# Performance work log

Hardware: AMD Instinct MI355X
Metric: run time of the kernel (lower is better)

The kernel has to match this reference:

```python
import jax, jax.numpy as jnp
import numpy as np

DEPTH = 2; C = 96; DIN = 192; R = 6; N = 16; K = 4
B = 1; H0 = 64; W0 = 64; L0 = H0 * W0


def layer_norm(x, g, b, eps=1e-5):
    m = jnp.mean(x, -1, keepdims=True)
    v = jnp.var(x, -1, keepdims=True)
    return (x - m) / jnp.sqrt(v + eps) * g + b


def selective_scan(u, delta, A, Bs, Cs, D):
    # u, delta: (B, KD, L); A: (KD, N); Bs, Cs: (B, K, N, L); D: (KD,)
    Bb, KD, L = u.shape
    Kk = Bs.shape[1]; Dd = KD // Kk; Nn = A.shape[1]
    dA = jnp.exp(delta[..., None] * A[None, :, None, :])              # (B,KD,L,N)
    Bfull = jnp.broadcast_to(Bs[:, :, None], (Bb, Kk, Dd, Nn, L)).reshape(Bb, KD, Nn, L)
    Cfull = jnp.broadcast_to(Cs[:, :, None], (Bb, Kk, Dd, Nn, L)).reshape(Bb, KD, Nn, L)
    dBu = delta[..., None] * Bfull.transpose(0, 1, 3, 2) * u[..., None]  # (B,KD,L,N)
    Ct = Cfull.transpose(3, 0, 1, 2)                                   # (L,B,KD,N)

    def step(h, inp):
        dA_t, dBu_t, C_t = inp
        h = dA_t * h + dBu_t
        return h, jnp.sum(h * C_t, -1)

    init = jnp.zeros((Bb, KD, Nn), u.dtype)
    _, ys = jax.lax.scan(step, init, (dA.transpose(2, 0, 1, 3), dBu.transpose(2, 0, 1, 3), Ct))
    y = ys.transpose(1, 2, 0)                                          # (B,KD,L)
    return y + D[None, :, None] * u


def ss2d(x, in_proj_w, conv_w, conv_b, x_proj_w, dt_w, dt_b, A_logs, Ds, outn_g, outn_b, out_proj_w):
    # x: (B,H,W,C)
    Bb, H, W, Cc = x.shape
    L = H * W
    xz = x @ in_proj_w.T                                  # (B,H,W,2*DIN)
    Din = xz.shape[-1] // 2
    xc, z = xz[..., :Din], xz[..., Din:]
    xc = xc.transpose(0, 3, 1, 2)                         # (B,DIN,H,W)
    xc = jax.lax.conv_general_dilated(xc, conv_w, (1, 1), 'SAME',
                                      feature_group_count=Din,
                                      dimension_numbers=('NCHW', 'OIHW', 'NCHW'))
    xc = jax.nn.silu(xc + conv_b[None, :, None, None])
    # cross-scan: 4 directions
    x0 = xc.reshape(Bb, Din, L)
    x1 = xc.transpose(0, 1, 3, 2).reshape(Bb, Din, L)
    xs = jnp.stack([x0, x1, jnp.flip(x0, -1), jnp.flip(x1, -1)], 1)  # (B,K,DIN,L)
    x_dbl = jnp.einsum('bkdl,kcd->bkcl', xs, x_proj_w)
    dts, Bm, Cm = x_dbl[:, :, :R], x_dbl[:, :, R:R + N], x_dbl[:, :, R + N:]
    dts = jnp.einsum('bkrl,kdr->bkdl', dts, dt_w)
    u = xs.reshape(Bb, K * Din, L)
    delta = jax.nn.softplus(dts.reshape(Bb, K * Din, L) + dt_b.reshape(K * Din)[None, :, None])
    A = -jnp.exp(A_logs)                                  # (K*DIN, N)
    ys = selective_scan(u, delta, A, Bm, Cm, Ds).reshape(Bb, K, Din, L)
    # cross-merge
    y0 = ys[:, 0]
    y1 = ys[:, 1].reshape(Bb, Din, W, H).transpose(0, 1, 3, 2).reshape(Bb, Din, L)
    y2 = jnp.flip(ys[:, 2], -1)
    y3 = jnp.flip(ys[:, 3], -1).reshape(Bb, Din, W, H).transpose(0, 1, 3, 2).reshape(Bb, Din, L)
    y = (y0 + y1 + y2 + y3).transpose(0, 2, 1).reshape(Bb, H, W, Din)
    y = layer_norm(y, outn_g, outn_b)
    y = y * jax.nn.silu(z)
    return y @ out_proj_w.T                               # (B,H,W,C)


def setup_inputs() -> dict:
    key = jax.random.key(0)
    ks = jax.random.split(key, 10)
    f = jnp.float32
    rn = lambda k, s: jax.random.normal(k, s, f) * 0.02
    return {
        'x': jax.random.normal(ks[0], (B, L0, C), f),
        'H': H0, 'W': W0,
        'norm1_g': jnp.ones((DEPTH, C), f), 'norm1_b': jnp.zeros((DEPTH, C), f),
        'vssn_g': jnp.ones((DEPTH, C), f), 'vssn_b': jnp.zeros((DEPTH, C), f),
        'in_proj_w': rn(ks[1], (DEPTH, 2 * DIN, C)),
        'conv_w': rn(ks[2], (DEPTH, DIN, 1, 3, 3)),
        'conv_b': jnp.zeros((DEPTH, DIN), f),
        'x_proj_w': rn(ks[3], (DEPTH, K, R + 2 * N, DIN)),
        'dt_w': rn(ks[4], (DEPTH, K, DIN, R)),
        'dt_b': jax.random.uniform(ks[5], (DEPTH, K, DIN), f, -4.0, -2.0),
        'A_logs': jnp.log(jnp.broadcast_to(jnp.arange(1, N + 1, dtype=f), (DEPTH, K * DIN, N))),
        'Ds': jnp.ones((DEPTH, K * DIN), f),
        'outn_g': jnp.ones((DEPTH, DIN), f), 'outn_b': jnp.zeros((DEPTH, DIN), f),
        'out_proj_w': rn(ks[6], (DEPTH, C, DIN)),
        'res_conv_w': rn(ks[7], (C, C, 3, 3)),
        'res_conv_b': jnp.zeros((C,), f),
    }


def reference(x, H, W, norm1_g, norm1_b, vssn_g, vssn_b, in_proj_w, conv_w, conv_b,
              x_proj_w, dt_w, dt_b, A_logs, Ds, outn_g, outn_b, out_proj_w,
              res_conv_w, res_conv_b):
    Bb, Ll, Cc = x.shape
    shortcut = x
    for i in range(DEPTH):
        sc = x
        xn = layer_norm(x, norm1_g[i], norm1_b[i]).reshape(Bb, H, W, Cc)
        # VSSBlock: internal pre-norm + residual around SS2D (drop_path = 0)
        xi = xn + ss2d(layer_norm(xn, vssn_g[i], vssn_b[i]), in_proj_w[i], conv_w[i],
                       conv_b[i], x_proj_w[i], dt_w[i], dt_b[i], A_logs[i], Ds[i],
                       outn_g[i], outn_b[i], out_proj_w[i])
        x = sc + xi.reshape(Bb, Ll, Cc)
    xc = x.transpose(0, 2, 1).reshape(Bb, Cc, H, W)
    xc = jax.lax.conv_general_dilated(xc, res_conv_w, (1, 1), 'SAME',
                                      dimension_numbers=('NCHW', 'OIHW', 'NCHW'))
    xc = xc + res_conv_b[None, :, None, None]
    return xc.reshape(Bb, Cc, Ll).transpose(0, 2, 1) + shortcut
```

## Files before the change

### kernel.cpp

```cpp
#include <hip/hip_runtime.h>
#include <math.h>

#define LTOK 4096
#define CCH  96
#define DIN_ 192
#define KDIR 4
#define NST  16
#define KD_  768

#define O_XN     0
#define O_XZ     786432
#define O_XCONV  2359296
#define O_XCONVT 3145728
#define O_DELTA  3932160
#define O_BM     7077888
#define O_CM     7340032
#define O_YS     9961472
#define O_XCUR   13107200

__device__ __forceinline__ float siluf(float x) { return x / (1.f + __expf(-x)); }

__global__ void fusedA_kernel(const float* __restrict__ x, const float* __restrict__ g1,
                              const float* __restrict__ b1, const float* __restrict__ g2,
                              const float* __restrict__ b2, const float* __restrict__ w,
                              float* __restrict__ xn, float* __restrict__ xz) {
  __shared__ float As[96 * 72];
  __shared__ float Bs[96 * 68];
  int tid = threadIdx.x;
  int l0 = blockIdx.x * 64;
  int j0 = blockIdx.y * 64;
  int m = tid >> 2, j = tid & 3;
  int l = l0 + m;
  float v[24];
  float s = 0.f, ss = 0.f;
#pragma unroll
  for (int t = 0; t < 24; ++t) {
    int k = j + 4 * t;
    float vv = x[l * 96 + k];
    v[t] = vv; s += vv; ss += vv * vv;
  }
  s += __shfl_xor(s, 1); ss += __shfl_xor(ss, 1);
  s += __shfl_xor(s, 2); ss += __shfl_xor(ss, 2);
  float m1 = s * (1.f / 96.f);
  float rs1 = rsqrtf(ss * (1.f / 96.f) - m1 * m1 + 1e-5f);
  float s2 = 0.f, ss2 = 0.f;
#pragma unroll
  for (int t = 0; t < 24; ++t) {
    int k = j + 4 * t;
    float nv = (v[t] - m1) * rs1 * g1[k] + b1[k];
    v[t] = nv; s2 += nv; ss2 += nv * nv;
    if (blockIdx.y == 0) xn[l * 96 + k] = nv;
  }
  s2 += __shfl_xor(s2, 1); ss2 += __shfl_xor(ss2, 1);
  s2 += __shfl_xor(s2, 2); ss2 += __shfl_xor(ss2, 2);
  float m2 = s2 * (1.f / 96.f);
  float rs2 = rsqrtf(ss2 * (1.f / 96.f) - m2 * m2 + 1e-5f);
#pragma unroll
  for (int t = 0; t < 24; ++t) {
    int k = j + 4 * t;
    As[k * 72 + m] = (v[t] - m2) * rs2 * g2[k] + b2[k];
  }
  for (int qi = tid; qi < 64 * 24; qi += 256) {
    int nn = qi / 24, q = qi % 24;
    const float4 wv = *(const float4*)&w[(j0 + nn) * 96 + q * 4];
    Bs[(q * 4 + 0) * 68 + nn] = wv.x;
    Bs[(q * 4 + 1) * 68 + nn] = wv.y;
    Bs[(q * 4 + 2) * 68 + nn] = wv.z;
    Bs[(q * 4 + 3) * 68 + nn] = wv.w;
  }
  __syncthreads();
  int mg = tid & 15, ng = tid >> 4;
  float acc[4][4] = {};
  for (int k = 0; k < 96; ++k) {
    float a0 = As[k * 72 + 4 * mg + 0], a1 = As[k * 72 + 4 * mg + 1];
    float a2 = As[k * 72 + 4 * mg + 2], a3 = As[k * 72 + 4 * mg + 3];
    float b0 = Bs[k * 68 + 4 * ng + 0], b1_ = Bs[k * 68 + 4 * ng + 1];
    float b2_ = Bs[k * 68 + 4 * ng + 2], b3 = Bs[k * 68 + 4 * ng + 3];
    acc[0][0] += a0 * b0; acc[0][1] += a0 * b1_; acc[0][2] += a0 * b2_; acc[0][3] += a0 * b3;
    acc[1][0] += a1 * b0; acc[1][1] += a1 * b1_; acc[1][2] += a1 * b2_; acc[1][3] += a1 * b3;
    acc[2][0] += a2 * b0; acc[2][1] += a2 * b1_; acc[2][2] += a2 * b2_; acc[2][3] += a2 * b3;
    acc[3][0] += a3 * b0; acc[3][1] += a3 * b1_; acc[3][2] += a3 * b2_; acc[3][3] += a3 * b3;
  }
#pragma unroll
  for (int i = 0; i < 4; ++i) {
    float4 o = make_float4(acc[i][0], acc[i][1], acc[i][2], acc[i][3]);
    *(float4*)&xz[(l0 + 4 * mg + i) * 384 + j0 + 4 * ng] = o;
  }
}

__global__ void dwconvT_kernel(const float* __restrict__ xz, const float* __restrict__ cw,
                               const float* __restrict__ cb, float* __restrict__ xconv,
                               float* __restrict__ xconvT) {
  int w0 = blockIdx.x * 16, h0 = blockIdx.y * 16, d0 = blockIdx.z * 8;
  __shared__ float xs[324 * 9];
  int tid = threadIdx.x;
  for (int idx = tid; idx < 324 * 8; idx += 256) {
    int dd = idx & 7;
    int p = idx >> 3;
    int ph = p / 18, pw = p - ph * 18;
    int hh = h0 + ph - 1, ww = w0 + pw - 1;
    float v = 0.f;
    if (hh >= 0 && hh < 64 && ww >= 0 && ww < 64) v = xz[(hh * 64 + ww) * 384 + d0 + dd];
    xs[p * 9 + dd] = v;
  }
  __syncthreads();
  int wi = tid & 15, hi = tid >> 4;
  for (int dd = 0; dd < 8; ++dd) {
    int d = d0 + dd;
    float acc = cb[d];
    const float* wgt = cw + d * 9;
#pragma unroll
    for (int r = 0; r < 3; ++r)
#pragma unroll
      for (int c = 0; c < 3; ++c)
        acc += xs[((hi + r) * 18 + wi + c) * 9 + dd] * wgt[r * 3 + c];
    float o = siluf(acc);
    xconv[d * LTOK + (h0 + hi) * 64 + w0 + wi] = o;
    xconvT[d * LTOK + (w0 + wi) * 64 + h0 + hi] = o;
  }
}

__global__ void projdelta_kernel(const float* __restrict__ xconv, const float* __restrict__ xconvT,
                                 const float* __restrict__ xpw, const float* __restrict__ dtw,
                                 const float* __restrict__ dtb, float* __restrict__ delta,
                                 float* __restrict__ Bm, float* __restrict__ Cm) {
  int chunk = blockIdx.x;
  int k = blockIdx.y;
  int l0 = chunk * 32;
  __shared__ float xsm[192 * 32];
  __shared__ float xdm[38 * 32];
  int tid = threadIdx.x;
  const float* ub = ((k & 1) ? xconvT : xconv);
  bool rev = (k >= 2);
  for (int idx = tid; idx < 192 * 32; idx += 256) {
    int i = idx & 31, d = idx >> 5;
    int l = l0 + i;
    xsm[idx] = ub[d * LTOK + (rev ? 4095 - l : l)];
  }
  __syncthreads();
  for (int o = tid; o < 38 * 32; o += 256) {
    int i = o & 31, c = o >> 5;
    const float* wr = xpw + (k * 38 + c) * 192;
    float acc = 0.f;
#pragma unroll 8
    for (int d = 0; d < 192; ++d) acc += wr[d] * xsm[d * 32 + i];
    xdm[o] = acc;
    if (c >= 6) {
      int l = l0 + i;
      if (c < 22) Bm[(k * LTOK + l) * NST + (c - 6)] = acc;
      else        Cm[(k * LTOK + l) * NST + (c - 22)] = acc;
    }
  }
  __syncthreads();
  for (int o = tid; o < 192 * 32; o += 256) {
    int i = o & 31, d = o >> 5;
    float acc = dtb[k * 192 + d];
    const float* wr = dtw + (k * 192 + d) * 6;
#pragma unroll
    for (int r = 0; r < 6; ++r) acc += xdm[r * 32 + i] * wr[r];
    float sp = (acc > 20.f) ? acc : log1pf(__expf(acc));
    delta[(k * 192 + d) * LTOK + l0 + i] = sp;
  }
}

__global__ __launch_bounds__(256) void scan_fused(
    const float* __restrict__ delta, const float* __restrict__ Bm,
    const float* __restrict__ Cm, const float* __restrict__ xconv,
    const float* __restrict__ xconvT, const float* __restrict__ A_logs,
    const float* __restrict__ Ds, float* __restrict__ ys) {
  int kd = blockIdx.x;
  int k = kd / 192, d = kd - k * 192;
  int tid = threadIdx.x;
  int nq = tid & 3;
  int c = tid >> 2;
  const float* ub = ((k & 1) ? xconvT : xconv) + d * LTOK;
  bool rev = (k >= 2);
  float A0 = -__expf(A_logs[kd * 16 + 4 * nq + 0]);
  float A1 = -__expf(A_logs[kd * 16 + 4 * nq + 1]);
  float A2 = -__expf(A_logs[kd * 16 + 4 * nq + 2]);
  float A3 = -__expf(A_logs[kd * 16 + 4 * nq + 3]);
  const float* dp = delta + kd * LTOK;
  const float* bp = Bm + k * LTOK * NST;
  const float* cp = Cm + k * LTOK * NST;
  __shared__ float Ps[16 * 65], Qs[16 * 65], H0s[16 * 65];
  int l0 = c * 64;
  float h0 = 0.f, h1 = 0.f, h2 = 0.f, h3 = 0.f;
  float P0 = 1.f, P1 = 1.f, P2 = 1.f, P3 = 1.f;
  for (int t = 0; t < 64; t += 4) {
    int l = l0 + t;
    float4 dlt4 = *(const float4*)(dp + l);
    float4 u4;
    if (!rev) u4 = *(const float4*)(ub + l);
    else { float4 tp = *(const float4*)(ub + 4092 - l); u4 = make_float4(tp.w, tp.z, tp.y, tp.x); }
#pragma unroll
    for (int s = 0; s < 4; ++s) {
      float dlt = (s == 0) ? dlt4.x : (s == 1) ? dlt4.y : (s == 2) ? dlt4.z : dlt4.w;
      float uu  = (s == 0) ? u4.x  : (s == 1) ? u4.y  : (s == 2) ? u4.z  : u4.w;
      float4 B4 = *(const float4*)(bp + (l + s) * NST + 4 * nq);
      float du = dlt * uu;
      float a0 = __expf(dlt * A0), a1 = __expf(dlt * A1);
      float a2 = __expf(dlt * A2), a3 = __expf(dlt * A3);
      h0 = a0 * h0 + du * B4.x; h1 = a1 * h1 + du * B4.y;
      h2 = a2 * h2 + du * B4.z; h3 = a3 * h3 + du * B4.w;
      P0 *= a0; P1 *= a1; P2 *= a2; P3 *= a3;
    }
  }
  Ps[(4 * nq + 0) * 65 + c] = P0; Qs[(4 * nq + 0) * 65 + c] = h0;
  Ps[(4 * nq + 1) * 65 + c] = P1; Qs[(4 * nq + 1) * 65 + c] = h1;
  Ps[(4 * nq + 2) * 65 + c] = P2; Qs[(4 * nq + 2) * 65 + c] = h2;
  Ps[(4 * nq + 3) * 65 + c] = P3; Qs[(4 * nq + 3) * 65 + c] = h3;
  __syncthreads();
  {
    int wv = tid >> 6, lane = tid & 63;
#pragma unroll
    for (int r = 0; r < 4; ++r) {
      int nn = wv * 4 + r;
      float P = Ps[nn * 65 + lane];
      float S = Qs[nn * 65 + lane];
#pragma unroll
      for (int off = 1; off < 64; off <<= 1) {
        float pp = __shfl_up(P, off);
        float sp = __shfl_up(S, off);
        if (lane >= off) { S = sp * P + S; P = pp * P; }
      }
      float g0 = __shfl_up(S, 1);
      if (lane == 0) g0 = 0.f;
      H0s[nn * 65 + lane] = g0;
    }
  }
  __syncthreads();
  float Dv = Ds[kd];
  float* yk = ys + (k * DIN_ + d) * LTOK;
  h0 = H0s[(4 * nq + 0) * 65 + c];
  h1 = H0s[(4 * nq + 1) * 65 + c];
  h2 = H0s[(4 * nq + 2) * 65 + c];
  h3 = H0s[(4 * nq + 3) * 65 + c];
  for (int t = 0; t < 64; t += 4) {
    int l = l0 + t;
    float4 dlt4 = *(const float4*)(dp + l);
    float4 u4;
    if (!rev) u4 = *(const float4*)(ub + l);
    else { float4 tp = *(const float4*)(ub + 4092 - l); u4 = make_float4(tp.w, tp.z, tp.y, tp.x); }
    float y4[4];
#pragma unroll
    for (int s = 0; s < 4; ++s) {
      float dlt = (s == 0) ? dlt4.x : (s == 1) ? dlt4.y : (s == 2) ? dlt4.z : dlt4.w;
      float uu  = (s == 0) ? u4.x  : (s == 1) ? u4.y  : (s == 2) ? u4.z  : u4.w;
      float4 B4 = *(const float4*)(bp + (l + s) * NST + 4 * nq);
      float4 C4 = *(const float4*)(cp + (l + s) * NST + 4 * nq);
      float du = dlt * uu;
      float a0 = __expf(dlt * A0), a1 = __expf(dlt * A1);
      float a2 = __expf(dlt * A2), a3 = __expf(dlt * A3);
      h0 = a0 * h0 + du * B4.x; h1 = a1 * h1 + du * B4.y;
      h2 = a2 * h2 + du * B4.z; h3 = a3 * h3 + du * B4.w;
      float p = h0 * C4.x + h1 * C4.y + h2 * C4.z + h3 * C4.w;
      p += __shfl_xor(p, 1);
      p += __shfl_xor(p, 2);
      y4[s] = p + Dv * uu;
    }
    if (nq == 0) {
      if (k == 0) {
        *(float4*)(yk + l) = make_float4(y4[0], y4[1], y4[2], y4[3]);
      } else if (k == 2) {
        *(float4*)(yk + 4092 - l) = make_float4(y4[3], y4[2], y4[1], y4[0]);
      } else if (k == 1) {
#pragma unroll
        for (int s = 0; s < 4; ++s) yk[(t + s) * 64 + c] = y4[s];
      } else {
#pragma unroll
        for (int s = 0; s < 4; ++s) yk[(63 - (t + s)) * 64 + (63 - c)] = y4[s];
      }
    }
  }
}

__global__ void combine_out(const float* __restrict__ ys, const float* __restrict__ xz,
                            const float* __restrict__ xn, const float* __restrict__ xsrc,
                            const float* __restrict__ og, const float* __restrict__ ob,
                            const float* __restrict__ ow, float* __restrict__ xout) {
  __shared__ float Ys[192 * 33];
  __shared__ float Bs[64 * 100];
  int tid = threadIdx.x;
  int l0 = blockIdx.x * 32;
  for (int it = tid; it < 192 * 8; it += 256) {
    int d = it >> 3, g = it & 7;
    int l = l0 + g * 4;
    float4 a0 = *(const float4*)&ys[(0 * DIN_ + d) * LTOK + l];
    float4 a1 = *(const float4*)&ys[(1 * DIN_ + d) * LTOK + l];
    float4 a2 = *(const float4*)&ys[(2 * DIN_ + d) * LTOK + l];
    float4 a3 = *(const float4*)&ys[(3 * DIN_ + d) * LTOK + l];
    float* yr = &Ys[d * 33 + g * 4];
    yr[0] = a0.x + a1.x + a2.x + a3.x;
    yr[1] = a0.y + a1.y + a2.y + a3.y;
    yr[2] = a0.z + a1.z + a2.z + a3.z;
    yr[3] = a0.w + a1.w + a2.w + a3.w;
  }
  __syncthreads();
  {
    int m = tid >> 3, q = tid & 7;
    int l = l0 + m;
    float zval[24];
    const float* zp = xz + l * 384 + 192 + q * 24;
#pragma unroll
    for (int i = 0; i < 6; ++i) {
      float4 zv = *(const float4*)(zp + 4 * i);
      zval[4 * i + 0] = zv.x; zval[4 * i + 1] = zv.y;
      zval[4 * i + 2] = zv.z; zval[4 * i + 3] = zv.w;
    }
    float s = 0.f, ssum = 0.f;
    float vv[24];
#pragma unroll
    for (int i = 0; i < 24; ++i) {
      float v = Ys[(q * 24 + i) * 33 + m];
      vv[i] = v; s += v; ssum += v * v;
    }
    s += __shfl_xor(s, 1); ssum += __shfl_xor(ssum, 1);
    s += __shfl_xor(s, 2); ssum += __shfl_xor(ssum, 2);
    s += __shfl_xor(s, 4); ssum += __shfl_xor(ssum, 4);
    float mu = s * (1.f / 192.f);
    float rs = rsqrtf(ssum * (1.f / 192.f) - mu * mu + 1e-5f);
#pragma unroll
    for (int i = 0; i < 24; ++i) {
      int d = q * 24 + i;
      float yn = (vv[i] - mu) * rs * og[d] + ob[d];
      Ys[d * 33 + m] = yn * siluf(zval[i]);
    }
  }
  int mg = tid & 31, cg = tid >> 5;
  float acc[12] = {};
  for (int kc = 0; kc < 3; ++kc) {
    __syncthreads();
    for (int qi = tid; qi < 96 * 16; qi += 256) {
      int cix = qi / 16, q = qi % 16;
      const float4 wv = *(const float4*)&ow[cix * 192 + kc * 64 + q * 4];
      Bs[(q * 4 + 0) * 100 + cix] = wv.x;
      Bs[(q * 4 + 1) * 100 + cix] = wv.y;
      Bs[(q * 4 + 2) * 100 + cix] = wv.z;
      Bs[(q * 4 + 3) * 100 + cix] = wv.w;
    }
    __syncthreads();
    for (int kk = 0; kk < 64; ++kk) {
      float a = Ys[(kc * 64 + kk) * 33 + mg];
      const float* br = &Bs[kk * 100 + cg * 12];
#pragma unroll
      for (int jj = 0; jj < 12; ++jj) acc[jj] += a * br[jj];
    }
  }
  int ll = l0 + mg;
#pragma unroll
  for (int jj = 0; jj < 12; ++jj) {
    int cix = cg * 12 + jj;
    xout[ll * 96 + cix] = xsrc[ll * 96 + cix] + xn[ll * 96 + cix] + acc[jj];
  }
}

__global__ void resconv_part(const float* __restrict__ x, const float* __restrict__ w,
                             float* __restrict__ pbuf) {
  int tile = blockIdx.x;
  int cs = blockIdx.y;
  int th0 = (tile >> 3) * 8, tw0 = (tile & 7) * 8;
  int cbase = cs * 6;
  __shared__ float xs[600];
  __shared__ float wlds[96 * 6 * 12];
  int tid = threadIdx.x;
  for (int idx = tid; idx < 600; idx += 256) {
    int cc = idx % 6;
    int pos = idx / 6;
    int hh = th0 + pos / 10 - 1;
    int ww = tw0 + pos % 10 - 1;
    float v = 0.f;
    if (hh >= 0 && hh < 64 && ww >= 0 && ww < 64) v = x[(hh * 64 + ww) * 96 + cbase + cc];
    xs[cc * 100 + pos] = v;
  }
  for (int idx = tid; idx < 96 * 54; idx += 256) {
    int c0 = idx / 54, o = idx - c0 * 54;
    int cc = o / 9, t = o - cc * 9;
    wlds[(c0 * 6 + cc) * 12 + t] = w[c0 * 864 + (cbase + cc) * 9 + t];
  }
  __syncthreads();
  int lane = tid & 63;
  int th = lane >> 3, tw = lane & 7;
  int c0g = tid >> 6;
  float acc[24] = {};
  for (int cc = 0; cc < 6; ++cc) {
    float xv[9];
#pragma unroll
    for (int r = 0; r < 3; ++r)
#pragma unroll
      for (int q = 0; q < 3; ++q) xv[r * 3 + q] = xs[cc * 100 + (th + r) * 10 + tw + q];
#pragma unroll
    for (int j = 0; j < 24; ++j) {
      const float* wr = &wlds[((c0g * 24 + j) * 6 + cc) * 12];
      float4 w0 = *(const float4*)wr;
      float4 w1 = *(const float4*)(wr + 4);
      float w8 = wr[8];
      acc[j] += xv[0] * w0.x + xv[1] * w0.y + xv[2] * w0.z + xv[3] * w0.w
              + xv[4] * w1.x + xv[5] * w1.y + xv[6] * w1.z + xv[7] * w1.w + xv[8] * w8;
    }
  }
  int l = (th0 + th) * 64 + tw0 + tw;
  float* pb = pbuf + cs * 393216 + l * 96 + c0g * 24;
#pragma unroll
  for (int j = 0; j < 24; j += 4)
    *(float4*)(pb + j) = make_float4(acc[j], acc[j + 1], acc[j + 2], acc[j + 3]);
}

__global__ void resconv_reduce(const float* __restrict__ pbuf, const float* __restrict__ b,
                               const float* __restrict__ shortcut, float* __restrict__ out) {
  int i4 = blockIdx.x * 256 + threadIdx.x;
  int base = i4 * 4;
  int c4 = base % 96;
  float4 s = *(const float4*)(shortcut + base);
  float4 bb = *(const float4*)(b + c4);
  s.x += bb.x; s.y += bb.y; s.z += bb.z; s.w += bb.w;
#pragma unroll
  for (int ss = 0; ss < 16; ++ss) {
    float4 p = *(const float4*)(pbuf + ss * 393216 + base);
    s.x += p.x; s.y += p.y; s.z += p.z; s.w += p.w;
  }
  *(float4*)(out + base) = s;
}

extern "C" void kernel_launch(void* const* d_in, const int* in_sizes, int n_in,
                              void* d_out, int out_size, void* d_ws, size_t ws_size,
                              hipStream_t stream) {
  const float* x_in     = (const float*)d_in[0];
  const float* norm1_g  = (const float*)d_in[3];
  const float* norm1_b  = (const float*)d_in[4];
  const float* vssn_g   = (const float*)d_in[5];
  const float* vssn_b   = (const float*)d_in[6];
  const float* in_proj  = (const float*)d_in[7];
  const float* conv_w   = (const float*)d_in[8];
  const float* conv_b   = (const float*)d_in[9];
  const float* x_proj   = (const float*)d_in[10];
  const float* dt_w     = (const float*)d_in[11];
  const float* dt_b     = (const float*)d_in[12];
  const float* A_logs   = (const float*)d_in[13];
  const float* Ds       = (const float*)d_in[14];
  const float* outn_g   = (const float*)d_in[15];
  const float* outn_b   = (const float*)d_in[16];
  const float* out_proj = (const float*)d_in[17];
  const float* rc_w     = (const float*)d_in[18];
  const float* rc_b     = (const float*)d_in[19];

  float* ws = (float*)d_ws;
  float* xn    = ws + O_XN;
  float* xz    = ws + O_XZ;
  float* xconv = ws + O_XCONV;
  float* xconvT= ws + O_XCONVT;
  float* delta = ws + O_DELTA;
  float* Bm    = ws + O_BM;
  float* Cm    = ws + O_CM;
  float* ysb   = ws + O_YS;
  float* xcur  = ws + O_XCUR;
  float* pbuf  = ws + O_DELTA;

  const float* xsrc = x_in;
  for (int i = 0; i < 2; ++i) {
    fusedA_kernel<<<dim3(64, 6), 256, 0, stream>>>(xsrc,
        norm1_g + i * 96, norm1_b + i * 96, vssn_g + i * 96, vssn_b + i * 96,
        in_proj + i * 36864, xn, xz);
    dwconvT_kernel<<<dim3(4, 4, 24), 256, 0, stream>>>(xz, conv_w + i * 1728,
        conv_b + i * 192, xconv, xconvT);
    projdelta_kernel<<<dim3(128, 4), 256, 0, stream>>>(xconv, xconvT,
        x_proj + i * 29184, dt_w + i * 4608, dt_b + i * 768, delta, Bm, Cm);
    scan_fused<<<768, 256, 0, stream>>>(delta, Bm, Cm, xconv, xconvT,
        A_logs + i * 12288, Ds + i * 768, ysb);
    combine_out<<<128, 256, 0, stream>>>(ysb, xz, xn, xsrc,
        outn_g + i * 192, outn_b + i * 192, out_proj + i * 18432, xcur);
    xsrc = xcur;
  }
  resconv_part<<<dim3(64, 16), 256, 0, stream>>>(xcur, rc_w, pbuf);
  resconv_reduce<<<384, 256, 0, stream>>>(pbuf, rc_b, x_in, (float*)d_out);
}
```

Measured before the change: 378.5 us.

## Tile x_proj GEMM in shared memory and widen scan to 512 threads

The projection/delta kernel now stages both the input chunk and the x_proj weights in shared memory with float4 loads, and each thread computes five output channels with 4-wide dot products. Reversed directions load contiguous natural-order data and mirror the index on output, which avoids per-element reversed gathers. The scan kernel splits the 16 states across 8 lanes of 2 states each instead of 4 lanes of 4, doubling the threads per block to expose more parallelism per chunk. This costs an extra shuffle reduction step and duplicated delta/u loads across lanes, in exchange for shorter per-thread dependency chains.

```diff
diff --git a/kernel.cpp b/kernel.cpp
--- a/kernel.cpp
+++ b/kernel.cpp
@@ -120,50 +120,76 @@
   }
 }
 
-__global__ void projdelta_kernel(const float* __restrict__ xconv, const float* __restrict__ xconvT,
-                                 const float* __restrict__ xpw, const float* __restrict__ dtw,
-                                 const float* __restrict__ dtb, float* __restrict__ delta,
-                                 float* __restrict__ Bm, float* __restrict__ Cm) {
+__global__ __launch_bounds__(256) void projdelta_kernel(
+    const float* __restrict__ xconv, const float* __restrict__ xconvT,
+    const float* __restrict__ xpw, const float* __restrict__ dtw,
+    const float* __restrict__ dtb, float* __restrict__ delta,
+    float* __restrict__ Bm, float* __restrict__ Cm) {
   int chunk = blockIdx.x;
   int k = blockIdx.y;
   int l0 = chunk * 32;
-  __shared__ float xsm[192 * 32];
-  __shared__ float xdm[38 * 32];
-  int tid = threadIdx.x;
+  bool rev = (k >= 2);
+  int lnat0 = rev ? (4064 - l0) : l0;
   const float* ub = ((k & 1) ? xconvT : xconv);
-  bool rev = (k >= 2);
-  for (int idx = tid; idx < 192 * 32; idx += 256) {
-    int i = idx & 31, d = idx >> 5;
-    int l = l0 + i;
-    xsm[idx] = ub[d * LTOK + (rev ? 4095 - l : l)];
-  }
-  __syncthreads();
-  for (int o = tid; o < 38 * 32; o += 256) {
-    int i = o & 31, c = o >> 5;
-    const float* wr = xpw + (k * 38 + c) * 192;
-    float acc = 0.f;
-#pragma unroll 8
-    for (int d = 0; d < 192; ++d) acc += wr[d] * xsm[d * 32 + i];
-    xdm[o] = acc;
-    if (c >= 6) {
-      int l = l0 + i;
-      if (c < 22) Bm[(k * LTOK + l) * NST + (c - 6)] = acc;
-      else        Cm[(k * LTOK + l) * NST + (c - 22)] = acc;
-    }
-  }
-  __syncthreads();
-  for (int o = tid; o < 192 * 32; o += 256) {
-    int i = o & 31, d = o >> 5;
-    float acc = dtb[k * 192 + d];
-    const float* wr = dtw + (k * 192 + d) * 6;
-#pragma unroll
-    for (int r = 0; r < 6; ++r) acc += xdm[r * 32 + i] * wr[r];
-    float sp = (acc > 20.f) ? acc : log1pf(__expf(acc));
-    delta[(k * 192 + d) * LTOK + l0 + i] = sp;
-  }
-}
-
-__global__ __launch_bounds__(256) void scan_fused(
+  __shared__ float Us[192 * 34];
+  __shared__ float Ws[38 * 196];
+  __shared__ float xdm[6 * 34];
+  int tid = threadIdx.x;
+  for (int idx = tid; idx < 192 * 8; idx += 256) {
+    int q = idx & 7, d = idx >> 3;
+    float4 v = *(const float4*)&ub[d * LTOK + lnat0 + 4 * q];
+    *(float4*)&Us[d * 34 + 4 * q] = v;
+  }
+  for (int idx = tid; idx < 38 * 48; idx += 256) {
+    int q = idx % 48, c = idx / 48;
+    float4 v = *(const float4*)&xpw[(k * 38 + c) * 192 + 4 * q];
+    *(float4*)&Ws[c * 196 + 4 * q] = v;
+  }
+  __syncthreads();
+  int ip = tid & 31;
+  int cg = tid >> 5;
+  int crow[5];
+#pragma unroll
+  for (int j = 0; j < 5; ++j) {
+    int c = cg * 5 + j;
+    crow[j] = ((c < 38) ? c : 0) * 196;
+  }
+  float acc[5] = {};
+  for (int d = 0; d < 192; d += 4) {
+    float u0 = Us[(d + 0) * 34 + ip];
+    float u1 = Us[(d + 1) * 34 + ip];
+    float u2 = Us[(d + 2) * 34 + ip];
+    float u3 = Us[(d + 3) * 34 + ip];
+#pragma unroll
+    for (int j = 0; j < 5; ++j) {
+      const float4 wv = *(const float4*)&Ws[crow[j] + d];
+      acc[j] += u0 * wv.x + u1 * wv.y + u2 * wv.z + u3 * wv.w;
+    }
+  }
+  int i = rev ? (31 - ip) : ip;
+  int l = l0 + i;
+#pragma unroll
+  for (int j = 0; j < 5; ++j) {
+    int c = cg * 5 + j;
+    if (c < 6)       xdm[c * 34 + ip] = acc[j];
+    else if (c < 22) Bm[((k << 12) + l) * NST + (c - 6)] = acc[j];
+    else if (c < 38) Cm[((k << 12) + l) * NST + (c - 22)] = acc[j];
+  }
+  __syncthreads();
+  const float* dtwk = dtw + k * 192 * 6;
+  const float* dtbk = dtb + k * 192;
+  int dg = tid >> 5;
+  for (int m = 0; m < 24; ++m) {
+    int d = dg + 8 * m;
+    float a = dtbk[d];
+#pragma unroll
+    for (int r = 0; r < 6; ++r) a += dtwk[d * 6 + r] * xdm[r * 34 + ip];
+    float sp = (a > 20.f) ? a : log1pf(__expf(a));
+    delta[(k * 192 + d) * LTOK + l] = sp;
+  }
+}
+
+__global__ __launch_bounds__(512) void scan_fused(
     const float* __restrict__ delta, const float* __restrict__ Bm,
     const float* __restrict__ Cm, const float* __restrict__ xconv,
     const float* __restrict__ xconvT, const float* __restrict__ A_logs,
@@ -171,21 +197,18 @@
   int kd = blockIdx.x;
   int k = kd / 192, d = kd - k * 192;
   int tid = threadIdx.x;
-  int nq = tid & 3;
-  int c = tid >> 2;
+  int nq = tid & 7;
+  int c = tid >> 3;
   const float* ub = ((k & 1) ? xconvT : xconv) + d * LTOK;
   bool rev = (k >= 2);
-  float A0 = -__expf(A_logs[kd * 16 + 4 * nq + 0]);
-  float A1 = -__expf(A_logs[kd * 16 + 4 * nq + 1]);
-  float A2 = -__expf(A_logs[kd * 16 + 4 * nq + 2]);
-  float A3 = -__expf(A_logs[kd * 16 + 4 * nq + 3]);
+  float A0 = -__expf(A_logs[kd * 16 + 2 * nq + 0]);
+  float A1 = -__expf(A_logs[kd * 16 + 2 * nq + 1]);
   const float* dp = delta + kd * LTOK;
   const float* bp = Bm + k * LTOK * NST;
   const float* cp = Cm + k * LTOK * NST;
   __shared__ float Ps[16 * 65], Qs[16 * 65], H0s[16 * 65];
   int l0 = c * 64;
-  float h0 = 0.f, h1 = 0.f, h2 = 0.f, h3 = 0.f;
-  float P0 = 1.f, P1 = 1.f, P2 = 1.f, P3 = 1.f;
+  float h0 = 0.f, h1 = 0.f, P0 = 1.f, P1 = 1.f;
   for (int t = 0; t < 64; t += 4) {
     int l = l0 + t;
     float4 dlt4 = *(const float4*)(dp + l);
@@ -196,25 +219,21 @@
     for (int s = 0; s < 4; ++s) {
       float dlt = (s == 0) ? dlt4.x : (s == 1) ? dlt4.y : (s == 2) ? dlt4.z : dlt4.w;
       float uu  = (s == 0) ? u4.x  : (s == 1) ? u4.y  : (s == 2) ? u4.z  : u4.w;
-      float4 B4 = *(const float4*)(bp + (l + s) * NST + 4 * nq);
+      float2 B2 = *(const float2*)(bp + (l + s) * NST + 2 * nq);
       float du = dlt * uu;
       float a0 = __expf(dlt * A0), a1 = __expf(dlt * A1);
-      float a2 = __expf(dlt * A2), a3 = __expf(dlt * A3);
-      h0 = a0 * h0 + du * B4.x; h1 = a1 * h1 + du * B4.y;
-      h2 = a2 * h2 + du * B4.z; h3 = a3 * h3 + du * B4.w;
-      P0 *= a0; P1 *= a1; P2 *= a2; P3 *= a3;
-    }
-  }
-  Ps[(4 * nq + 0) * 65 + c] = P0; Qs[(4 * nq + 0) * 65 + c] = h0;
-  Ps[(4 * nq + 1) * 65 + c] = P1; Qs[(4 * nq + 1) * 65 + c] = h1;
-  Ps[(4 * nq + 2) * 65 + c] = P2; Qs[(4 * nq + 2) * 65 + c] = h2;
-  Ps[(4 * nq + 3) * 65 + c] = P3; Qs[(4 * nq + 3) * 65 + c] = h3;
+      h0 = a0 * h0 + du * B2.x; h1 = a1 * h1 + du * B2.y;
+      P0 *= a0; P1 *= a1;
+    }
+  }
+  Ps[(2 * nq + 0) * 65 + c] = P0; Qs[(2 * nq + 0) * 65 + c] = h0;
+  Ps[(2 * nq + 1) * 65 + c] = P1; Qs[(2 * nq + 1) * 65 + c] = h1;
   __syncthreads();
   {
     int wv = tid >> 6, lane = tid & 63;
 #pragma unroll
-    for (int r = 0; r < 4; ++r) {
-      int nn = wv * 4 + r;
+    for (int r = 0; r < 2; ++r) {
+      int nn = wv * 2 + r;
       float P = Ps[nn * 65 + lane];
       float S = Qs[nn * 65 + lane];
 #pragma unroll
@@ -231,10 +250,8 @@
   __syncthreads();
   float Dv = Ds[kd];
   float* yk = ys + (k * DIN_ + d) * LTOK;
-  h0 = H0s[(4 * nq + 0) * 65 + c];
-  h1 = H0s[(4 * nq + 1) * 65 + c];
-  h2 = H0s[(4 * nq + 2) * 65 + c];
-  h3 = H0s[(4 * nq + 3) * 65 + c];
+  h0 = H0s[(2 * nq + 0) * 65 + c];
+  h1 = H0s[(2 * nq + 1) * 65 + c];
   for (int t = 0; t < 64; t += 4) {
     int l = l0 + t;
     float4 dlt4 = *(const float4*)(dp + l);
@@ -246,16 +263,15 @@
     for (int s = 0; s < 4; ++s) {
       float dlt = (s == 0) ? dlt4.x : (s == 1) ? dlt4.y : (s == 2) ? dlt4.z : dlt4.w;
       float uu  = (s == 0) ? u4.x  : (s == 1) ? u4.y  : (s == 2) ? u4.z  : u4.w;
-      float4 B4 = *(const float4*)(bp + (l + s) * NST + 4 * nq);
-      float4 C4 = *(const float4*)(cp + (l + s) * NST + 4 * nq);
+      float2 B2 = *(const float2*)(bp + (l + s) * NST + 2 * nq);
+      float2 C2 = *(const float2*)(cp + (l + s) * NST + 2 * nq);
       float du = dlt * uu;
       float a0 = __expf(dlt * A0), a1 = __expf(dlt * A1);
-      float a2 = __expf(dlt * A2), a3 = __expf(dlt * A3);
-      h0 = a0 * h0 + du * B4.x; h1 = a1 * h1 + du * B4.y;
-      h2 = a2 * h2 + du * B4.z; h3 = a3 * h3 + du * B4.w;
-      float p = h0 * C4.x + h1 * C4.y + h2 * C4.z + h3 * C4.w;
+      h0 = a0 * h0 + du * B2.x; h1 = a1 * h1 + du * B2.y;
+      float p = h0 * C2.x + h1 * C2.y;
       p += __shfl_xor(p, 1);
       p += __shfl_xor(p, 2);
+      p += __shfl_xor(p, 4);
       y4[s] = p + Dv * uu;
     }
     if (nq == 0) {
@@ -464,7 +480,7 @@
         conv_b + i * 192, xconv, xconvT);
     projdelta_kernel<<<dim3(128, 4), 256, 0, stream>>>(xconv, xconvT,
         x_proj + i * 29184, dt_w + i * 4608, dt_b + i * 768, delta, Bm, Cm);
-    scan_fused<<<768, 256, 0, stream>>>(delta, Bm, Cm, xconv, xconvT,
+    scan_fused<<<768, 512, 0, stream>>>(delta, Bm, Cm, xconv, xconvT,
         A_logs + i * 12288, Ds + i * 768, ysb);
     combine_out<<<128, 256, 0, stream>>>(ysb, xz, xn, xsrc,
         outn_g + i * 192, outn_b + i * 192, out_proj + i * 18432, xcur);
```

Result: no change. 381.0 us (+0.7%).
